# Kernel tuning notes

Hardware: AMD Instinct MI355X
Metric: run time of the kernel (lower is better)

Reference implementation:

```python
import jax, jax.numpy as jnp
from jax import lax
import numpy as np

B = 512

def setup_inputs() -> dict:
    key = jax.random.key(0)
    ks = jax.random.split(key, 6)
    x = jax.random.normal(ks[0], (B, 1, 28, 28), jnp.float32)
    conv1_w = jax.random.normal(ks[1], (256, 1, 9, 9), jnp.float32) * 0.05
    conv1_b = jnp.zeros((256,), jnp.float32)
    prim_w = jax.random.normal(ks[2], (32, 32, 1, 9, 9), jnp.float32) * 0.02
    prim_b = jnp.zeros((32,), jnp.float32)
    dig_W = jax.random.normal(ks[3], (1152, 8, 16), jnp.float32) * 0.1
    dig_Wb = jnp.zeros((1152, 16), jnp.float32)
    out_w = jax.random.normal(ks[4], (10, 10, 16, 1), jnp.float32) * 0.1
    out_b = jnp.zeros((10,), jnp.float32)
    return dict(x=x, conv1_w=conv1_w, conv1_b=conv1_b, prim_w=prim_w, prim_b=prim_b,
                dig_W=dig_W, dig_Wb=dig_Wb, out_w=out_w, out_b=out_b)


def _squash(s):
    # s: [B, 16, 10]; matches torch: v = ||s||_2/(1+||s||_2) * (s^T / ||s||_1)
    l2 = jnp.sqrt(jnp.sum(s * s, axis=1))[:, :, None]      # [B, 10, 1]
    l1 = jnp.sum(jnp.abs(s), axis=1)[:, :, None]            # [B, 10, 1]
    return l2 / (1.0 + l2) * (jnp.swapaxes(s, 1, 2) / l1)   # [B, 10, 16]


def reference(x, conv1_w, conv1_b, prim_w, prim_b, dig_W, dig_Wb, out_w, out_b):
    # conv1: [B,1,28,28] -> [B,256,20,20]
    out = lax.conv_general_dilated(x, conv1_w, (1, 1), 'VALID',
                                   dimension_numbers=('NCHW', 'OIHW', 'NCHW'))
    out = jax.nn.relu(out + conv1_b[None, :, None, None])
    # primary capsules: [B,32,8,20,20] -> [B,32,8,6,6]
    out1 = out.reshape(-1, 32, 8, 20, 20)
    out1 = lax.conv_general_dilated(out1, prim_w, (1, 2, 2), 'VALID',
                                    dimension_numbers=('NCDHW', 'OIDHW', 'NCDHW'))
    out1 = jax.nn.relu(out1 + prim_b[None, :, None, None, None])
    # transpose(2,-1) then reshape -> [B, 1152, 8]
    u = jnp.swapaxes(out1, 2, 4).reshape(-1, 1152, 8)
    # per-capsule affine: [B,1152,16]
    dig = jnp.einsum('bnd,nde->bne', u, dig_W) + dig_Wb
    bsz = dig.shape[0]
    # dynamic routing: b logits are never updated in the source, so
    # c = softmax(zeros, dim=1) = 1/1152 uniform, and all 3 iterations produce
    # the identical v. Computed once (same math as the original loop).
    c = jnp.full((bsz, 1152, 10), 1.0 / 1152, dtype=dig.dtype)
    s = jnp.einsum('bni,bnd->bdi', c, dig)   # [B, 16, 10]
    v = _squash(s)                            # [B, 10, 16]
    # output Conv2d(10,10,[16,1]) on v[...,None] reduces fully -> [B,10]
    logits = jnp.einsum('bik,oik->bo', v, out_w[..., 0]) + out_b
    return jax.nn.softmax(logits, axis=1)
```

## Files before the change

### kernel.cpp

```cpp
#include <hip/hip_runtime.h>
#include <math.h>


typedef __attribute__((ext_vector_type(8))) short bf16x8;
typedef __attribute__((ext_vector_type(4))) float f32x4;

__device__ inline unsigned short f2bf(float f) {
    union { float f; unsigned u; } v; v.f = f;
    unsigned r = v.u + 0x7fff + ((v.u >> 16) & 1);
    return (unsigned short)(r >> 16);
}

#define C1TN 16008

__global__ void caps_pre(const float* __restrict__ conv1_w,
                         const float* __restrict__ prim_w,
                         const float* __restrict__ dig_Wb,
                         const float* __restrict__ out_w,
                         float* __restrict__ S,
                         float* __restrict__ colsum,
                         float* __restrict__ OW,
                         unsigned short* __restrict__ c1wp2,
                         unsigned short* __restrict__ pw2,
                         int B)
{
    const int t = threadIdx.x;
    if (blockIdx.x == 468) {
        __shared__ float cs[16];
        if (t < 16) cs[t] = 0.f;
        __syncthreads();
        {
            const int k = t & 15, g = t >> 4;
            float s = 0.f;
            for (int j = 0; j < 72; ++j) s += dig_Wb[(g * 72 + j) * 16 + k];
            atomicAdd(&cs[k], s);
        }
        __syncthreads();
        if (t < 16) colsum[t] = cs[t];
        if (t >= 64 && t < 224) {
            const int idx = t - 64, o = idx >> 4, k = idx & 15;
            float s = 0.f;
            for (int i = 0; i < 10; ++i) s += out_w[(o * 10 + i) * 16 + k];
            OW[idx] = s;
        }
        return;
    }
    const int tid = blockIdx.x * 256 + t;
    if (tid < 24576) {
        const int c = tid / 96, kn = tid % 96;
        unsigned short v = 0;
        if (kn < 72) {
            const int p = kn >> 1, lo = kn & 1, ky = p >> 2, kx = 2 * (p & 3) + lo;
            v = f2bf(conv1_w[c * 81 + 9 * ky + kx]);
        } else if (kn < 81) {
            v = f2bf(conv1_w[c * 81 + 9 * (kn - 72) + 8]);
        }
        c1wp2[tid] = v;
    } else if (tid < 24576 + 87040) {
        const int j = tid - 24576;
        const int t81 = j >> 10, rem = j & 1023, o = rem >> 5, i = rem & 31;
        pw2[j] = (t81 < 81) ? f2bf(prim_w[(o * 32 + i) * 81 + t81]) : (unsigned short)0;
    } else {
        const int k = tid - 111616;
        if (k < B * 16) S[k] = 0.f;
    }
}

__global__ __launch_bounds__(256, 2) void caps_main(
    const float* __restrict__ x,
    const float* __restrict__ conv1_b,
    const float* __restrict__ prim_b,
    const float* __restrict__ dig_W,
    const unsigned short* __restrict__ c1wp2,
    const unsigned short* __restrict__ pw2,
    float* __restrict__ S)
{
    __shared__ __align__(16) unsigned short c1t[2 * C1TN];
    __shared__ __align__(16) unsigned imgp[1344];
    __shared__ unsigned short offT[64];
    __shared__ float pbs[32];

    const int b = blockIdx.x >> 2, dp = blockIdx.x & 3;
    const int d0 = dp * 2;
    const int t = threadIdx.x;
    const int wave = t >> 6, lane = t & 63, quad = lane >> 4, l16 = lane & 15;

    const float* xb = x + b * 784;
    for (int j = t; j < 1344; j += 256) {
        unsigned v = 0;
        if (j < 784) {
            const float a = xb[j];
            const int xc = j - 28 * (int)(((unsigned)j * 37450u) >> 20);
            const float c = (xc < 27) ? xb[j + 1] : 0.f;
            v = (unsigned)f2bf(a) | ((unsigned)f2bf(c) << 16);
        }
        imgp[j] = v;
    }
    if (t < 64) {
        int v;
        if (t < 32) {
            const int ky = t >> 2, kx = 2 * (t & 3);
            v = ky * 28 + kx;
        } else {
            const int k = t + 32;
            if (k < 72) {
                const int p = k >> 1, lo = k & 1, ky = p >> 2, kx = 2 * (p & 3) + lo;
                v = ky * 28 + kx;
            } else if (k < 81) {
                v = (k - 72) * 28 + 8;
            } else v = 784;
        }
        offT[t] = (unsigned short)(4 * v);
    }
    if (t < 32) pbs[t] = prim_b[t];
    __syncthreads();

    unsigned tp0[4], tp1[4], t2a[4], t2b[4];
#pragma unroll
    for (int r = 0; r < 4; ++r) {
        tp0[r] = offT[quad * 4 + r];
        tp1[r] = offT[16 + quad * 4 + r];
        t2a[r] = offT[32 + quad * 8 + 2 * r];
        t2b[r] = offT[32 + quad * 8 + 2 * r + 1];
    }

    {
        const int e = wave >> 1;
        const int d = d0 + e;
        unsigned short* dst = c1t + e * C1TN;
        const float cb0 = conv1_b[l16 * 8 + d];
        const float cb1 = conv1_b[(16 + l16) * 8 + d];
        bf16x8 Bw0[3], Bw1[3];
#pragma unroll
        for (int ks = 0; ks < 3; ++ks) {
            Bw0[ks] = *(const bf16x8*)&c1wp2[(l16 * 8 + d) * 96 + ks * 32 + quad * 8];
            Bw1[ks] = *(const bf16x8*)&c1wp2[((16 + l16) * 8 + d) * 96 + ks * 32 + quad * 8];
        }
        for (int mt = (wave & 1); mt < 25; mt += 2) {
            const int pos = mt * 16 + l16;
            const int y = (int)(((unsigned)pos * 52429u) >> 20);
            const unsigned pb4 = (unsigned)(pos + 8 * y) * 4u;
            f32x4 a0 = {0.f, 0.f, 0.f, 0.f}, a1 = {0.f, 0.f, 0.f, 0.f};
            union { unsigned u[4]; bf16x8 v; } A;
#pragma unroll
            for (int r = 0; r < 4; ++r)
                A.u[r] = *(const unsigned*)((const char*)imgp + (pb4 + tp0[r]));
            a0 = __builtin_amdgcn_mfma_f32_16x16x32_bf16(A.v, Bw0[0], a0, 0, 0, 0);
            a1 = __builtin_amdgcn_mfma_f32_16x16x32_bf16(A.v, Bw1[0], a1, 0, 0, 0);
#pragma unroll
            for (int r = 0; r < 4; ++r)
                A.u[r] = *(const unsigned*)((const char*)imgp + (pb4 + tp1[r]));
            a0 = __builtin_amdgcn_mfma_f32_16x16x32_bf16(A.v, Bw0[1], a0, 0, 0, 0);
            a1 = __builtin_amdgcn_mfma_f32_16x16x32_bf16(A.v, Bw1[1], a1, 0, 0, 0);
#pragma unroll
            for (int r = 0; r < 4; ++r) {
                const unsigned lo = *(const unsigned*)((const char*)imgp + (pb4 + t2a[r]));
                const unsigned hi = *(const unsigned*)((const char*)imgp + (pb4 + t2b[r]));
                A.u[r] = (lo & 0xFFFFu) | (hi << 16);
            }
            a0 = __builtin_amdgcn_mfma_f32_16x16x32_bf16(A.v, Bw0[2], a0, 0, 0, 0);
            a1 = __builtin_amdgcn_mfma_f32_16x16x32_bf16(A.v, Bw1[2], a1, 0, 0, 0);
#pragma unroll
            for (int r = 0; r < 4; ++r) {
                const int pr = mt * 16 + quad * 4 + r;
                const int spar = (int)((((unsigned)pr * 52429u) >> 21) & 1u);
                const int base = pr * 40 + 8 * spar;
                dst[base + l16]      = f2bf(fmaxf(a0[r] + cb0, 0.f));
                dst[base + 16 + l16] = f2bf(fmaxf(a1[r] + cb1, 0.f));
            }
        }
    }
    __syncthreads();

    const int hp = l16 >> 3, wp = l16 & 7;
    const unsigned Lbase = 80u * (unsigned)(40 * hp + 2 * wp) + 16u * quad;
    const unsigned Lh0 = Lbase + 16u * hp;
    const unsigned Lh1 = Lbase + 16u * (1 - hp);

    f32x4 pa[12];
#pragma unroll
    for (int q = 0; q < 12; ++q) pa[q] = (f32x4){0.f, 0.f, 0.f, 0.f};

    {
        const unsigned short* apbase = pw2 + l16 * 32 + quad * 8;
        int off = wave;
        bf16x8 A0 = *(const bf16x8*)(apbase + off * 1024);
        bf16x8 A1 = *(const bf16x8*)(apbase + off * 1024 + 512);
        for (; off < 81; off += 4) {
            const int noff = off + 4;
            const bf16x8 nA0 = *(const bf16x8*)(apbase + noff * 1024);
            const bf16x8 nA1 = *(const bf16x8*)(apbase + noff * 1024 + 512);
            const int ky = (off * 57) >> 9;
            const int kx = off - 9 * ky;
            const int kk = (ky >> 1) & 1;
            const unsigned soff = 80u * (unsigned)(20 * ky + kx);
            const unsigned ad = (kk ? Lh1 : Lh0) + soff;
            const char* b0 = (const char*)c1t + ad;
#pragma unroll
            for (int nt = 0; nt < 3; ++nt) {
                const bf16x8 Bf0 = *(const bf16x8*)(b0 + nt * 6400);
                const bf16x8 Bf1 = *(const bf16x8*)(b0 + nt * 6400 + 2 * C1TN);
                pa[nt]     = __builtin_amdgcn_mfma_f32_16x16x32_bf16(A0, Bf0, pa[nt],     0, 0, 0);
                pa[3 + nt] = __builtin_amdgcn_mfma_f32_16x16x32_bf16(A1, Bf0, pa[3 + nt], 0, 0, 0);
                pa[6 + nt] = __builtin_amdgcn_mfma_f32_16x16x32_bf16(A0, Bf1, pa[6 + nt], 0, 0, 0);
                pa[9 + nt] = __builtin_amdgcn_mfma_f32_16x16x32_bf16(A1, Bf1, pa[9 + nt], 0, 0, 0);
            }
            A0 = nA0; A1 = nA1;
        }
    }
    __syncthreads();

    f32x4* redbuf = (f32x4*)c1t;
    if (wave >= 2) {
#pragma unroll
        for (int q = 0; q < 12; ++q) redbuf[((wave - 2) * 12 + q) * 64 + lane] = pa[q];
    }
    __syncthreads();
    if (wave < 2) {
#pragma unroll
        for (int q = 0; q < 12; ++q) pa[q] += redbuf[(wave * 12 + q) * 64 + lane];
        if (wave == 0) {
#pragma unroll
            for (int q = 0; q < 6; ++q) redbuf[(24 + q) * 64 + lane] = pa[6 + q];
        } else {
#pragma unroll
            for (int q = 0; q < 6; ++q) redbuf[(30 + q) * 64 + lane] = pa[q];
        }
    }
    __syncthreads();

    if (wave < 2) {
        const int d = d0 + wave;
        f32x4 full[6];
#pragma unroll
        for (int q = 0; q < 6; ++q)
            full[q] = (wave == 0) ? (pa[q] + redbuf[(30 + q) * 64 + lane])
                                  : (pa[6 + q] + redbuf[(24 + q) * 64 + lane]);

        float part[16];
#pragma unroll
        for (int k = 0; k < 16; ++k) part[k] = 0.f;

        if (wp < 6) {
#pragma unroll
            for (int mt = 0; mt < 2; ++mt)
#pragma unroll
                for (int nt = 0; nt < 3; ++nt) {
                    const f32x4 u4 = full[mt * 3 + nt];
                    const int h = 2 * nt + hp;
#pragma unroll
                    for (int r = 0; r < 4; ++r) {
                        const int o = mt * 16 + quad * 4 + r;
                        const float val = fmaxf(u4[r] + pbs[o], 0.f);
                        const int nc = o * 36 + wp * 6 + h;
                        const f32x4* wd = (const f32x4*)&dig_W[(nc * 8 + d) * 16];
#pragma unroll
                        for (int m = 0; m < 4; ++m) {
                            const f32x4 wv = wd[m];
                            part[m * 4 + 0] = fmaf(val, wv[0], part[m * 4 + 0]);
                            part[m * 4 + 1] = fmaf(val, wv[1], part[m * 4 + 1]);
                            part[m * 4 + 2] = fmaf(val, wv[2], part[m * 4 + 2]);
                            part[m * 4 + 3] = fmaf(val, wv[3], part[m * 4 + 3]);
                        }
                    }
                }
        }

#pragma unroll
        for (int k = 0; k < 16; ++k) {
            float v = part[k];
            v += __shfl_xor(v, 32, 64);
            v += __shfl_xor(v, 16, 64);
            v += __shfl_xor(v, 8, 64);
            v += __shfl_xor(v, 4, 64);
            v += __shfl_xor(v, 2, 64);
            v += __shfl_xor(v, 1, 64);
            part[k] = v;
        }
        if (lane == 0) {
#pragma unroll
            for (int k = 0; k < 16; ++k) atomicAdd(&S[b * 16 + k], part[k]);
        }
    }
}

__global__ void caps_epi(const float* __restrict__ S, const float* __restrict__ colsum,
                         const float* __restrict__ OW, const float* __restrict__ out_b,
                         float* __restrict__ out, int B)
{
    const int b = blockIdx.x * 256 + threadIdx.x;
    if (b >= B) return;
    float Sv[16]; float l2 = 0.f, l1 = 0.f;
#pragma unroll
    for (int k = 0; k < 16; ++k) {
        const float s = (S[b * 16 + k] + colsum[k]) * (1.f / 1152.f);
        Sv[k] = s; l2 += s * s; l1 += fabsf(s);
    }
    l2 = sqrtf(l2);
    const float sc = l2 / (1.f + l2) / l1;
    float lg[10]; float mx = -1e30f;
#pragma unroll
    for (int o = 0; o < 10; ++o) {
        float a = out_b[o];
#pragma unroll
        for (int k = 0; k < 16; ++k) a = fmaf(Sv[k] * sc, OW[o * 16 + k], a);
        lg[o] = a; mx = fmaxf(mx, a);
    }
    float sum = 0.f;
#pragma unroll
    for (int o = 0; o < 10; ++o) { lg[o] = expf(lg[o] - mx); sum += lg[o]; }
    const float inv = 1.f / sum;
#pragma unroll
    for (int o = 0; o < 10; ++o) out[b * 10 + o] = lg[o] * inv;
}

extern "C" void kernel_launch(void* const* d_in, const int* in_sizes, int n_in,
                              void* d_out, int out_size, void* d_ws, size_t ws_size,
                              hipStream_t stream) {
    const float* x       = (const float*)d_in[0];
    const float* conv1_w = (const float*)d_in[1];
    const float* conv1_b = (const float*)d_in[2];
    const float* prim_w  = (const float*)d_in[3];
    const float* prim_b  = (const float*)d_in[4];
    const float* dig_W   = (const float*)d_in[5];
    const float* dig_Wb  = (const float*)d_in[6];
    const float* out_w   = (const float*)d_in[7];
    const float* out_b   = (const float*)d_in[8];
    float* out = (float*)d_out;

    const int B = in_sizes[0] / 784;

    char* w = (char*)d_ws;
    float* S              = (float*)(w);
    float* colsum         = (float*)(w + 32768);
    float* OW             = (float*)(w + 32832);
    unsigned short* c1wp2 = (unsigned short*)(w + 33472);
    unsigned short* pw2   = (unsigned short*)(w + 33472 + 49152);

    caps_pre<<<469, 256, 0, stream>>>(conv1_w, prim_w, dig_Wb, out_w,
                                      S, colsum, OW, c1wp2, pw2, B);
    caps_main<<<B * 4, 256, 0, stream>>>(x, conv1_b, prim_b, dig_W, c1wp2, pw2, S);
    caps_epi<<<(B + 255) / 256, 256, 0, stream>>>(S, colsum, OW, out_b, out, B);
}
```

Before: 182.1 us.

## Split main kernel to one depth slice per block and fuse epilogue via last-block

Each main-kernel block now handles a single capsule depth slice instead of two. This halves shared memory and accumulator registers, allows 4 blocks per CU and launches twice as many blocks. The separate epilogue kernel is removed: a global done counter lets the last finishing block compute squash, logits and softmax for all batches. The prim weight repacking is also rewritten to read prim_w coalesced. The cost is that each image is now recomputed 8 times instead of 4 for the conv1 setup. The last-block epilogue runs serially in one block and hardcodes 512 batches.

Measured after the change: 422.0 us. +131.7%, slower.

```diff
diff --git a/kernel.cpp b/kernel.cpp
--- a/kernel.cpp
+++ b/kernel.cpp
@@ -20,6 +20,7 @@
                          float* __restrict__ S,
                          float* __restrict__ colsum,
                          float* __restrict__ OW,
+                         unsigned* __restrict__ done,
                          unsigned short* __restrict__ c1wp2,
                          unsigned short* __restrict__ pw2,
                          int B)
@@ -28,6 +29,7 @@
     if (blockIdx.x == 468) {
         __shared__ float cs[16];
         if (t < 16) cs[t] = 0.f;
+        if (t == 255) *done = 0u;
         __syncthreads();
         {
             const int k = t & 15, g = t >> 4;
@@ -56,32 +58,40 @@
             v = f2bf(conv1_w[c * 81 + 9 * (kn - 72) + 8]);
         }
         c1wp2[tid] = v;
-    } else if (tid < 24576 + 87040) {
+    } else if (tid < 107520) {
         const int j = tid - 24576;
-        const int t81 = j >> 10, rem = j & 1023, o = rem >> 5, i = rem & 31;
-        pw2[j] = (t81 < 81) ? f2bf(prim_w[(o * 32 + i) * 81 + t81]) : (unsigned short)0;
+        const int row = j / 81, tap = j - 81 * row;
+        pw2[tap * 1024 + row] = f2bf(prim_w[j]);
+    } else if (tid < 111616) {
+        pw2[81 * 1024 + (tid - 107520)] = 0;
     } else {
         const int k = tid - 111616;
         if (k < B * 16) S[k] = 0.f;
     }
 }
 
-__global__ __launch_bounds__(256, 2) void caps_main(
+__global__ __launch_bounds__(256, 4) void caps_main(
     const float* __restrict__ x,
     const float* __restrict__ conv1_b,
     const float* __restrict__ prim_b,
     const float* __restrict__ dig_W,
     const unsigned short* __restrict__ c1wp2,
     const unsigned short* __restrict__ pw2,
-    float* __restrict__ S)
+    float* __restrict__ S,
+    const float* __restrict__ colsum,
+    const float* __restrict__ OW,
+    const float* __restrict__ out_b,
+    unsigned* __restrict__ done,
+    float* __restrict__ out,
+    int nblocks)
 {
-    __shared__ __align__(16) unsigned short c1t[2 * C1TN];
+    __shared__ __align__(16) unsigned short c1t[C1TN];
     __shared__ __align__(16) unsigned imgp[1344];
     __shared__ unsigned short offT[64];
     __shared__ float pbs[32];
-
-    const int b = blockIdx.x >> 2, dp = blockIdx.x & 3;
-    const int d0 = dp * 2;
+    __shared__ int lastflag;
+
+    const int b = blockIdx.x >> 3, d = blockIdx.x & 7;
     const int t = threadIdx.x;
     const int wave = t >> 6, lane = t & 63, quad = lane >> 4, l16 = lane & 15;
 
@@ -113,6 +123,7 @@
         offT[t] = (unsigned short)(4 * v);
     }
     if (t < 32) pbs[t] = prim_b[t];
+    if (t == 0) lastflag = 0;
     __syncthreads();
 
     unsigned tp0[4], tp1[4], t2a[4], t2b[4];
@@ -125,9 +136,6 @@
     }
 
     {
-        const int e = wave >> 1;
-        const int d = d0 + e;
-        unsigned short* dst = c1t + e * C1TN;
         const float cb0 = conv1_b[l16 * 8 + d];
         const float cb1 = conv1_b[(16 + l16) * 8 + d];
         bf16x8 Bw0[3], Bw1[3];
@@ -136,7 +144,7 @@
             Bw0[ks] = *(const bf16x8*)&c1wp2[(l16 * 8 + d) * 96 + ks * 32 + quad * 8];
             Bw1[ks] = *(const bf16x8*)&c1wp2[((16 + l16) * 8 + d) * 96 + ks * 32 + quad * 8];
         }
-        for (int mt = (wave & 1); mt < 25; mt += 2) {
+        for (int mt = wave; mt < 25; mt += 4) {
             const int pos = mt * 16 + l16;
             const int y = (int)(((unsigned)pos * 52429u) >> 20);
             const unsigned pb4 = (unsigned)(pos + 8 * y) * 4u;
@@ -165,8 +173,8 @@
                 const int pr = mt * 16 + quad * 4 + r;
                 const int spar = (int)((((unsigned)pr * 52429u) >> 21) & 1u);
                 const int base = pr * 40 + 8 * spar;
-                dst[base + l16]      = f2bf(fmaxf(a0[r] + cb0, 0.f));
-                dst[base + 16 + l16] = f2bf(fmaxf(a1[r] + cb1, 0.f));
+                c1t[base + l16]      = f2bf(fmaxf(a0[r] + cb0, 0.f));
+                c1t[base + 16 + l16] = f2bf(fmaxf(a1[r] + cb1, 0.f));
             }
         }
     }
@@ -177,9 +185,9 @@
     const unsigned Lh0 = Lbase + 16u * hp;
     const unsigned Lh1 = Lbase + 16u * (1 - hp);
 
-    f32x4 pa[12];
-#pragma unroll
-    for (int q = 0; q < 12; ++q) pa[q] = (f32x4){0.f, 0.f, 0.f, 0.f};
+    f32x4 pa[6];
+#pragma unroll
+    for (int q = 0; q < 6; ++q) pa[q] = (f32x4){0.f, 0.f, 0.f, 0.f};
 
     {
         const unsigned short* apbase = pw2 + l16 * 32 + quad * 8;
@@ -199,11 +207,8 @@
 #pragma unroll
             for (int nt = 0; nt < 3; ++nt) {
                 const bf16x8 Bf0 = *(const bf16x8*)(b0 + nt * 6400);
-                const bf16x8 Bf1 = *(const bf16x8*)(b0 + nt * 6400 + 2 * C1TN);
                 pa[nt]     = __builtin_amdgcn_mfma_f32_16x16x32_bf16(A0, Bf0, pa[nt],     0, 0, 0);
                 pa[3 + nt] = __builtin_amdgcn_mfma_f32_16x16x32_bf16(A1, Bf0, pa[3 + nt], 0, 0, 0);
-                pa[6 + nt] = __builtin_amdgcn_mfma_f32_16x16x32_bf16(A0, Bf1, pa[6 + nt], 0, 0, 0);
-                pa[9 + nt] = __builtin_amdgcn_mfma_f32_16x16x32_bf16(A1, Bf1, pa[9 + nt], 0, 0, 0);
             }
             A0 = nA0; A1 = nA1;
         }
@@ -213,29 +218,28 @@
     f32x4* redbuf = (f32x4*)c1t;
     if (wave >= 2) {
 #pragma unroll
-        for (int q = 0; q < 12; ++q) redbuf[((wave - 2) * 12 + q) * 64 + lane] = pa[q];
+        for (int q = 0; q < 6; ++q) redbuf[((wave - 2) * 6 + q) * 64 + lane] = pa[q];
     }
     __syncthreads();
     if (wave < 2) {
 #pragma unroll
-        for (int q = 0; q < 12; ++q) pa[q] += redbuf[(wave * 12 + q) * 64 + lane];
+        for (int q = 0; q < 6; ++q) pa[q] += redbuf[(wave * 6 + q) * 64 + lane];
         if (wave == 0) {
 #pragma unroll
-            for (int q = 0; q < 6; ++q) redbuf[(24 + q) * 64 + lane] = pa[6 + q];
+            for (int q = 0; q < 3; ++q) redbuf[(12 + q) * 64 + lane] = pa[3 + q];
         } else {
 #pragma unroll
-            for (int q = 0; q < 6; ++q) redbuf[(30 + q) * 64 + lane] = pa[q];
+            for (int q = 0; q < 3; ++q) redbuf[(15 + q) * 64 + lane] = pa[q];
         }
     }
     __syncthreads();
 
     if (wave < 2) {
-        const int d = d0 + wave;
-        f32x4 full[6];
-#pragma unroll
-        for (int q = 0; q < 6; ++q)
-            full[q] = (wave == 0) ? (pa[q] + redbuf[(30 + q) * 64 + lane])
-                                  : (pa[6 + q] + redbuf[(24 + q) * 64 + lane]);
+        f32x4 full[3];
+#pragma unroll
+        for (int q = 0; q < 3; ++q)
+            full[q] = (wave == 0) ? (pa[q] + redbuf[(15 + q) * 64 + lane])
+                                  : (pa[3 + q] + redbuf[(12 + q) * 64 + lane]);
 
         float part[16];
 #pragma unroll
@@ -243,27 +247,25 @@
 
         if (wp < 6) {
 #pragma unroll
-            for (int mt = 0; mt < 2; ++mt)
-#pragma unroll
-                for (int nt = 0; nt < 3; ++nt) {
-                    const f32x4 u4 = full[mt * 3 + nt];
-                    const int h = 2 * nt + hp;
-#pragma unroll
-                    for (int r = 0; r < 4; ++r) {
-                        const int o = mt * 16 + quad * 4 + r;
-                        const float val = fmaxf(u4[r] + pbs[o], 0.f);
-                        const int nc = o * 36 + wp * 6 + h;
-                        const f32x4* wd = (const f32x4*)&dig_W[(nc * 8 + d) * 16];
-#pragma unroll
-                        for (int m = 0; m < 4; ++m) {
-                            const f32x4 wv = wd[m];
-                            part[m * 4 + 0] = fmaf(val, wv[0], part[m * 4 + 0]);
-                            part[m * 4 + 1] = fmaf(val, wv[1], part[m * 4 + 1]);
-                            part[m * 4 + 2] = fmaf(val, wv[2], part[m * 4 + 2]);
-                            part[m * 4 + 3] = fmaf(val, wv[3], part[m * 4 + 3]);
-                        }
+            for (int nt = 0; nt < 3; ++nt) {
+                const f32x4 u4 = full[nt];
+                const int h = 2 * nt + hp;
+#pragma unroll
+                for (int r = 0; r < 4; ++r) {
+                    const int o = wave * 16 + quad * 4 + r;
+                    const float val = fmaxf(u4[r] + pbs[o], 0.f);
+                    const int nc = o * 36 + wp * 6 + h;
+                    const f32x4* wd = (const f32x4*)&dig_W[(nc * 8 + d) * 16];
+#pragma unroll
+                    for (int m = 0; m < 4; ++m) {
+                        const f32x4 wv = wd[m];
+                        part[m * 4 + 0] = fmaf(val, wv[0], part[m * 4 + 0]);
+                        part[m * 4 + 1] = fmaf(val, wv[1], part[m * 4 + 1]);
+                        part[m * 4 + 2] = fmaf(val, wv[2], part[m * 4 + 2]);
+                        part[m * 4 + 3] = fmaf(val, wv[3], part[m * 4 + 3]);
                     }
                 }
+            }
         }
 
 #pragma unroll
@@ -280,38 +282,43 @@
         if (lane == 0) {
 #pragma unroll
             for (int k = 0; k < 16; ++k) atomicAdd(&S[b * 16 + k], part[k]);
-        }
-    }
-}
-
-__global__ void caps_epi(const float* __restrict__ S, const float* __restrict__ colsum,
-                         const float* __restrict__ OW, const float* __restrict__ out_b,
-                         float* __restrict__ out, int B)
-{
-    const int b = blockIdx.x * 256 + threadIdx.x;
-    if (b >= B) return;
-    float Sv[16]; float l2 = 0.f, l1 = 0.f;
-#pragma unroll
-    for (int k = 0; k < 16; ++k) {
-        const float s = (S[b * 16 + k] + colsum[k]) * (1.f / 1152.f);
-        Sv[k] = s; l2 += s * s; l1 += fabsf(s);
-    }
-    l2 = sqrtf(l2);
-    const float sc = l2 / (1.f + l2) / l1;
-    float lg[10]; float mx = -1e30f;
-#pragma unroll
-    for (int o = 0; o < 10; ++o) {
-        float a = out_b[o];
-#pragma unroll
-        for (int k = 0; k < 16; ++k) a = fmaf(Sv[k] * sc, OW[o * 16 + k], a);
-        lg[o] = a; mx = fmaxf(mx, a);
-    }
-    float sum = 0.f;
-#pragma unroll
-    for (int o = 0; o < 10; ++o) { lg[o] = expf(lg[o] - mx); sum += lg[o]; }
-    const float inv = 1.f / sum;
-#pragma unroll
-    for (int o = 0; o < 10; ++o) out[b * 10 + o] = lg[o] * inv;
+            __threadfence();
+        }
+    }
+    __syncthreads();
+
+    if (t == 0) {
+        const unsigned old = atomicAdd(done, 1u);
+        lastflag = (old == (unsigned)(nblocks - 1)) ? 1 : 0;
+    }
+    __syncthreads();
+    if (lastflag) {
+        __threadfence();
+        for (int bb = t; bb < 512; bb += 256) {
+            float Sv[16]; float l2 = 0.f, l1 = 0.f;
+#pragma unroll
+            for (int k = 0; k < 16; ++k) {
+                const float s = (S[bb * 16 + k] + colsum[k]) * (1.f / 1152.f);
+                Sv[k] = s; l2 += s * s; l1 += fabsf(s);
+            }
+            l2 = sqrtf(l2);
+            const float sc = l2 / (1.f + l2) / l1;
+            float lg[10]; float mx = -1e30f;
+#pragma unroll
+            for (int o = 0; o < 10; ++o) {
+                float a = out_b[o];
+#pragma unroll
+                for (int k = 0; k < 16; ++k) a = fmaf(Sv[k] * sc, OW[o * 16 + k], a);
+                lg[o] = a; mx = fmaxf(mx, a);
+            }
+            float sum = 0.f;
+#pragma unroll
+            for (int o = 0; o < 10; ++o) { lg[o] = expf(lg[o] - mx); sum += lg[o]; }
+            const float inv = 1.f / sum;
+#pragma unroll
+            for (int o = 0; o < 10; ++o) out[bb * 10 + o] = lg[o] * inv;
+        }
+    }
 }
 
 extern "C" void kernel_launch(void* const* d_in, const int* in_sizes, int n_in,
@@ -334,11 +341,13 @@
     float* S              = (float*)(w);
     float* colsum         = (float*)(w + 32768);
     float* OW             = (float*)(w + 32832);
-    unsigned short* c1wp2 = (unsigned short*)(w + 33472);
-    unsigned short* pw2   = (unsigned short*)(w + 33472 + 49152);
-
+    unsigned* done        = (unsigned*)(w + 33472);
+    unsigned short* c1wp2 = (unsigned short*)(w + 33536);
+    unsigned short* pw2   = (unsigned short*)(w + 33536 + 49152);
+
+    const int nblocks = B * 8;
     caps_pre<<<469, 256, 0, stream>>>(conv1_w, prim_w, dig_Wb, out_w,
-                                      S, colsum, OW, c1wp2, pw2, B);
-    caps_main<<<B * 4, 256, 0, stream>>>(x, conv1_b, prim_b, dig_W, c1wp2, pw2, S);
-    caps_epi<<<(B + 255) / 256, 256, 0, stream>>>(S, colsum, OW, out_b, out, B);
+                                      S, colsum, OW, done, c1wp2, pw2, B);
+    caps_main<<<nblocks, 256, 0, stream>>>(x, conv1_b, prim_b, dig_W, c1wp2, pw2,
+                                           S, colsum, OW, out_b, done, out, nblocks);
 }
```
